# Performance work log

Measured on AMD Instinct MI355X. Metric: run time of the kernel, lower is better.

The kernel has to match this reference:

```python
import jax, jax.numpy as jnp
import numpy as np

C = 256
NH = 8
G = 32  # groupnorm groups (min(32, C))
EPS = 1e-6


def setup_inputs() -> dict:
    key = jax.random.key(0)
    ks = jax.random.split(key, 7)
    B, D, H, W = 2, 16, 16, 16
    x = jax.random.normal(ks[0], (B, C, D, H, W), dtype=jnp.float32)
    gn_gamma = jnp.ones((C,), jnp.float32)
    gn_beta = jnp.zeros((C,), jnp.float32)
    s = 1.0 / np.sqrt(C)
    qkv_w = jax.random.normal(ks[1], (3 * C, C), jnp.float32) * s  # 1x1x1 conv weight
    qkv_b = jnp.zeros((3 * C,), jnp.float32)
    proj_w = jax.random.normal(ks[2], (C, C), jnp.float32) * s
    proj_b = jnp.zeros((C,), jnp.float32)
    return {"x": x, "gn_gamma": gn_gamma, "gn_beta": gn_beta,
            "qkv_w": qkv_w, "qkv_b": qkv_b, "proj_w": proj_w, "proj_b": proj_b}


def _group_norm(x, gamma, beta):
    # x: [B, C, S]
    B, Cc, S = x.shape
    xg = x.reshape(B, G, (Cc // G) * S)
    mu = xg.mean(axis=-1, keepdims=True)
    var = xg.var(axis=-1, keepdims=True)
    xg = (xg - mu) * jax.lax.rsqrt(var + EPS)
    x = xg.reshape(B, Cc, S)
    return x * gamma[None, :, None] + beta[None, :, None]


def reference(x, gn_gamma, gn_beta, qkv_w, qkv_b, proj_w, proj_b):
    B, Cc, D, H, W = x.shape
    S = D * H * W
    hd = Cc // NH
    xf = x.reshape(B, Cc, S)
    h = _group_norm(xf, gn_gamma, gn_beta)
    # 1x1x1 conv == channel matmul: [B, 3C, S]
    qkv = jnp.einsum('oc,bcs->bos', qkv_w, h) + qkv_b[None, :, None]
    # torch path: reshape(B,3C,S).permute(0,2,1).chunk -> q=channels[0:C]
    q, k, v = qkv[:, :Cc], qkv[:, Cc:2 * Cc], qkv[:, 2 * Cc:]
    # [B, C, S] -> [B, NH, S, hd]
    def to_heads(t):
        return t.reshape(B, NH, hd, S).transpose(0, 1, 3, 2)
    q, k, v = to_heads(q), to_heads(k), to_heads(v)
    scale = hd ** (-0.5)
    attn = jax.nn.softmax(jnp.einsum('bnqd,bnkd->bnqk', q, k) * scale, axis=-1)
    o = jnp.einsum('bnqk,bnkd->bnqd', attn, v)  # [B, NH, S, hd]
    o = o.transpose(0, 1, 3, 2).reshape(B, Cc, S)  # back to [B, C, S]
    o = jnp.einsum('oc,bcs->bos', proj_w, o) + proj_b[None, :, None]
    return x + o.reshape(B, Cc, D, H, W)
```

## Files before the change

kernel.cpp:

```cpp
#include <hip/hip_runtime.h>
#include <cstddef>

#define S_LEN 4096
#define C_DIM 256
#define NHEADS 8
#define HDIM 32

typedef __attribute__((ext_vector_type(8))) _Float16 half8;
typedef __attribute__((ext_vector_type(4))) _Float16 half4;
typedef __attribute__((ext_vector_type(2))) _Float16 h2t;
typedef __attribute__((ext_vector_type(2))) __fp16 fp16x2;
typedef __attribute__((ext_vector_type(4))) float floatx4;

#define SC2F ((float)(0.17677669529663687 * 1.4426950408889634))

__global__ __launch_bounds__(256) void prep_stats(
    const float* __restrict__ qkv_w, const float* __restrict__ proj_w,
    const float* __restrict__ qkv_b, const float* __restrict__ x,
    _Float16* __restrict__ wq, _Float16* __restrict__ wp,
    float* __restrict__ qbias, float* __restrict__ pstat)
{
  const int blk = blockIdx.x;
  const int tid = threadIdx.x;
  if (blk < 512) {
    __shared__ float red[2][4];
    const int gb = blk >> 3, e = blk & 7;
    const int g = gb & 31, b = gb >> 5;
    const float* xb = x + ((size_t)b * C_DIM + g * 8) * S_LEN + e * 4096;
    const float4* x4 = (const float4*)xb;
    float sum = 0.f, sumsq = 0.f;
    #pragma unroll
    for (int i = 0; i < 4; ++i) {
      float4 v = x4[tid + i * 256];
      sum += v.x + v.y + v.z + v.w;
      sumsq += v.x * v.x + v.y * v.y + v.z * v.z + v.w * v.w;
    }
    for (int off = 1; off < 64; off <<= 1) {
      sum += __shfl_xor(sum, off, 64);
      sumsq += __shfl_xor(sumsq, off, 64);
    }
    const int wv = tid >> 6, lane = tid & 63;
    if (lane == 0) { red[0][wv] = sum; red[1][wv] = sumsq; }
    __syncthreads();
    if (tid == 0) {
      pstat[(gb * 8 + e) * 2 + 0] = red[0][0] + red[0][1] + red[0][2] + red[0][3];
      pstat[(gb * 8 + e) * 2 + 1] = red[1][0] + red[1][1] + red[1][2] + red[1][3];
    }
  } else if (blk < 704) {
    const int i = (blk - 512) * 1024 + tid * 4;
    float4 v = *(const float4*)(qkv_w + i);
    const float sc = (i < 65536) ? SC2F : 1.f;
    half4 h = { (_Float16)(v.x * sc), (_Float16)(v.y * sc),
                (_Float16)(v.z * sc), (_Float16)(v.w * sc) };
    *(half4*)(wq + i) = h;
  } else if (blk < 768) {
    const int i = (blk - 704) * 1024 + tid * 4;
    float4 v = *(const float4*)(proj_w + i);
    half4 h = { (_Float16)v.x, (_Float16)v.y, (_Float16)v.z, (_Float16)v.w };
    *(half4*)(wp + i) = h;
  } else {
    #pragma unroll
    for (int j = 0; j < 3; ++j) {
      const int i = tid + j * 256;
      float bv = qkv_b[i];
      if (i < 256) bv *= SC2F;
      qbias[i] = bv;
    }
  }
}

__global__ __launch_bounds__(256) void xnorm(
    const float* __restrict__ x, const float* __restrict__ gamma,
    const float* __restrict__ beta, const float* __restrict__ pstat,
    _Float16* __restrict__ xt)
{
  __shared__ _Float16 Lt[16][264];
  const int tid = threadIdx.x;
  const int b = blockIdx.y;
  const int s0 = blockIdx.x * 16;
  const int c = tid;
  const int gb = b * 32 + (c >> 3);
  float s = 0.f, sq = 0.f;
  #pragma unroll
  for (int e = 0; e < 8; ++e) {
    s  += pstat[(gb * 8 + e) * 2 + 0];
    sq += pstat[(gb * 8 + e) * 2 + 1];
  }
  const float mean = s * (1.f / 32768.f);
  const float rstd = rsqrtf(sq * (1.f / 32768.f) - mean * mean + 1e-6f);
  const float ga = gamma[c] * rstd, be = beta[c] - mean * ga;
  const float4* xa = (const float4*)(x + ((size_t)b * C_DIM + c) * S_LEN + s0);
  #pragma unroll
  for (int i = 0; i < 4; ++i) {
    float4 v = xa[i];
    Lt[i * 4 + 0][c] = (_Float16)(v.x * ga + be);
    Lt[i * 4 + 1][c] = (_Float16)(v.y * ga + be);
    Lt[i * 4 + 2][c] = (_Float16)(v.z * ga + be);
    Lt[i * 4 + 3][c] = (_Float16)(v.w * ga + be);
  }
  __syncthreads();
  const int sl = tid >> 4, cc = (tid & 15) * 16;
  _Float16* dst = xt + ((size_t)b * S_LEN + s0 + sl) * C_DIM + cc;
  const _Float16* src = &Lt[sl][cc];
  *(half8*)(dst + 0) = *(const half8*)(src + 0);
  *(half8*)(dst + 8) = *(const half8*)(src + 8);
}

__global__ __launch_bounds__(256) void qkv_gemm(
    const _Float16* __restrict__ W, const float* __restrict__ bias,
    const _Float16* __restrict__ xt,
    _Float16* __restrict__ qo, _Float16* __restrict__ ko_,
    _Float16* __restrict__ vo)
{
  __shared__ __align__(16) _Float16 Ld[256 * 72];
  const int tid = threadIdx.x;
  const int b = blockIdx.z;
  const int s0 = blockIdx.y * 64;

  {
    const int sl = tid >> 2, cc = (tid & 3) * 64;
    const _Float16* src = xt + ((size_t)b * S_LEN + s0 + sl) * C_DIM + cc;
    _Float16* dst = &Ld[sl * 264 + cc];
    #pragma unroll
    for (int j = 0; j < 8; ++j)
      *(half8*)(dst + j * 8) = *(const half8*)(src + j * 8);
  }
  __syncthreads();

  const int lane = tid & 63, wv = tid >> 6;
  const int m = lane & 15, quad = lane >> 4;
  const int mtb = blockIdx.x * 16 + wv * 4;
  const _Float16* wrow[4];
  #pragma unroll
  for (int j = 0; j < 4; ++j)
    wrow[j] = W + (size_t)((mtb + j) * 16 + m) * C_DIM + quad * 8;
  const _Float16* lp = &Ld[m * 264 + quad * 8];

  floatx4 acc[4][4];
  #pragma unroll
  for (int j = 0; j < 4; ++j)
    #pragma unroll
    for (int s = 0; s < 4; ++s) acc[j][s] = (floatx4){0.f,0.f,0.f,0.f};

  #pragma unroll 2
  for (int k0 = 0; k0 < C_DIM; k0 += 32) {
    half8 b0 = *(const half8*)(lp + k0);
    half8 b1 = *(const half8*)(lp + 16 * 264 + k0);
    half8 b2 = *(const half8*)(lp + 32 * 264 + k0);
    half8 b3 = *(const half8*)(lp + 48 * 264 + k0);
    #pragma unroll
    for (int j = 0; j < 4; ++j) {
      half8 a = *(const half8*)(wrow[j] + k0);
      acc[j][0] = __builtin_amdgcn_mfma_f32_16x16x32_f16(a, b0, acc[j][0], 0, 0, 0);
      acc[j][1] = __builtin_amdgcn_mfma_f32_16x16x32_f16(a, b1, acc[j][1], 0, 0, 0);
      acc[j][2] = __builtin_amdgcn_mfma_f32_16x16x32_f16(a, b2, acc[j][2], 0, 0, 0);
      acc[j][3] = __builtin_amdgcn_mfma_f32_16x16x32_f16(a, b3, acc[j][3], 0, 0, 0);
    }
  }

  if (blockIdx.x < 2) {
    #pragma unroll
    for (int j = 0; j < 4; ++j) {
      const int ob = (mtb + j) * 16 + quad * 4;
      const float bv0 = bias[ob], bv1 = bias[ob + 1],
                  bv2 = bias[ob + 2], bv3 = bias[ob + 3];
      _Float16* dst = (ob < 256) ? qo : ko_;
      const int oo = ob & 255, n = oo >> 5, d0 = oo & 31;
      #pragma unroll
      for (int sub = 0; sub < 4; ++sub) {
        int s = s0 + sub * 16 + m;
        half4 h = { (_Float16)(acc[j][sub][0] + bv0), (_Float16)(acc[j][sub][1] + bv1),
                    (_Float16)(acc[j][sub][2] + bv2), (_Float16)(acc[j][sub][3] + bv3) };
        *(half4*)(dst + (((size_t)b * NHEADS + n) * S_LEN + s) * HDIM + d0) = h;
      }
    }
  } else {
    __syncthreads();
    _Float16* VLd = Ld;
    #pragma unroll
    for (int j = 0; j < 4; ++j) {
      const int ob = (mtb + j) * 16 + quad * 4;
      const int lch = (wv * 4 + j) * 16 + quad * 4;
      const float bv0 = bias[ob], bv1 = bias[ob + 1],
                  bv2 = bias[ob + 2], bv3 = bias[ob + 3];
      #pragma unroll
      for (int sub = 0; sub < 4; ++sub) {
        int s = sub * 16 + m;
        VLd[(lch + 0) * 72 + s] = (_Float16)(acc[j][sub][0] + bv0);
        VLd[(lch + 1) * 72 + s] = (_Float16)(acc[j][sub][1] + bv1);
        VLd[(lch + 2) * 72 + s] = (_Float16)(acc[j][sub][2] + bv2);
        VLd[(lch + 3) * 72 + s] = (_Float16)(acc[j][sub][3] + bv3);
      }
    }
    __syncthreads();
    const int sh3 = tid & 7, chl = tid >> 3;
    #pragma unroll
    for (int p = 0; p < 8; ++p) {
      const int ch = p * 32 + chl;
      const int n = ch >> 5, d = ch & 31;
      _Float16* dst = vo + ((size_t)(b * NHEADS + n) * HDIM + d) * S_LEN + s0 + sh3 * 8;
      *(half8*)dst = *(const half8*)(VLd + ch * 72 + sh3 * 8);
    }
  }
}

__global__ __launch_bounds__(512) void attn_kernel(
    const _Float16* __restrict__ q, const _Float16* __restrict__ k,
    const _Float16* __restrict__ v, _Float16* __restrict__ o)
{
  __shared__ __align__(16) _Float16 Kl[2][128 * 40];
  __shared__ __align__(16) _Float16 Vl[2][32 * 136];
  const int tid = threadIdx.x;
  const int lane = tid & 63, wv = tid >> 6;
  const int m = lane & 15, quad = lane >> 4;
  const int n = blockIdx.y, b = blockIdx.z;
  const int qc = blockIdx.x;
  const int q0 = qc * 256 + wv * 32;
  const int bh = b * NHEADS + n;

  const _Float16* qb = q + (size_t)bh * S_LEN * HDIM;
  const _Float16* kb = k + (size_t)bh * S_LEN * HDIM;
  const _Float16* vb = v + (size_t)bh * HDIM * S_LEN;

  half8 qfA = *(const half8*)(qb + (size_t)(q0 + m) * HDIM + quad * 8);
  half8 qfB = *(const half8*)(qb + (size_t)(q0 + 16 + m) * HDIM + quad * 8);

  const int krow = wv * 16 + (lane >> 2), kc = (lane & 3) * 8;
  const int vrow = wv * 4 + (lane >> 4), vc = (lane & 15) * 8;
  const _Float16* kg = kb + (size_t)krow * HDIM + kc;
  const _Float16* vg = vb + (size_t)vrow * S_LEN + vc;
  const int klds = krow * 40 + kc;
  const int vlds = vrow * 136 + vc;

  int4 kreg = *(const int4*)kg;
  int4 vreg = *(const int4*)vg;
  const _Float16* kgp = kg + 128 * HDIM;
  const _Float16* vgp = vg + 128;

  floatx4 oA0 = {0.f,0.f,0.f,0.f}, oA1 = oA0, oB0 = oA0, oB1 = oA0;
  float lA0 = 0.f, lA1 = 0.f, lB0 = 0.f, lB1 = 0.f;
  const fp16x2 one2 = { (__fp16)1.0f, (__fp16)1.0f };
  const floatx4 zz = {0.f,0.f,0.f,0.f};

  #pragma unroll 2
  for (int it = 0; it < 32; ++it) {
    const int bufi = it & 1;
    *(int4*)(&Kl[bufi][klds]) = kreg;
    *(int4*)(&Vl[bufi][vlds]) = vreg;
    kreg = *(const int4*)kgp; kgp += 128 * HDIM;
    vreg = *(const int4*)vgp; vgp += 128;
    __syncthreads();
    const _Float16* Kb = Kl[bufi];
    const _Float16* Vb = Vl[bufi];

    #pragma unroll
    for (int t = 0; t < 8; ++t) {
      const int tt = (t + wv) & 7;
      half8 kf  = *(const half8*)(Kb + (tt * 16 + m) * 40 + quad * 8);
      half4 vf0 = *(const half4*)(Vb + m * 136 + tt * 16 + quad * 4);
      half4 vf1 = *(const half4*)(Vb + (16 + m) * 136 + tt * 16 + quad * 4);
      __builtin_amdgcn_s_setprio(1);
      floatx4 sA = __builtin_amdgcn_mfma_f32_16x16x32_f16(kf, qfA, zz, 0, 0, 0);
      floatx4 sB = __builtin_amdgcn_mfma_f32_16x16x32_f16(kf, qfB, zz, 0, 0, 0);
      __builtin_amdgcn_s_setprio(0);
      float eA0 = __builtin_amdgcn_exp2f(sA[0]);
      float eA1 = __builtin_amdgcn_exp2f(sA[1]);
      float eA2 = __builtin_amdgcn_exp2f(sA[2]);
      float eA3 = __builtin_amdgcn_exp2f(sA[3]);
      float eB0 = __builtin_amdgcn_exp2f(sB[0]);
      float eB1 = __builtin_amdgcn_exp2f(sB[1]);
      float eB2 = __builtin_amdgcn_exp2f(sB[2]);
      float eB3 = __builtin_amdgcn_exp2f(sB[3]);
      half4 pA, pB;
      fp16x2 pAlo = __builtin_amdgcn_cvt_pkrtz(eA0, eA1);
      fp16x2 pAhi = __builtin_amdgcn_cvt_pkrtz(eA2, eA3);
      fp16x2 pBlo = __builtin_amdgcn_cvt_pkrtz(eB0, eB1);
      fp16x2 pBhi = __builtin_amdgcn_cvt_pkrtz(eB2, eB3);
      *(fp16x2*)&pA = pAlo; *((fp16x2*)&pA + 1) = pAhi;
      *(fp16x2*)&pB = pBlo; *((fp16x2*)&pB + 1) = pBhi;
      lA0 = __builtin_amdgcn_fdot2(pAlo, one2, lA0, false);
      lA1 = __builtin_amdgcn_fdot2(pAhi, one2, lA1, false);
      lB0 = __builtin_amdgcn_fdot2(pBlo, one2, lB0, false);
      lB1 = __builtin_amdgcn_fdot2(pBhi, one2, lB1, false);
      __builtin_amdgcn_s_setprio(1);
      oA0 = __builtin_amdgcn_mfma_f32_16x16x16f16(vf0, pA, oA0, 0, 0, 0);
      oA1 = __builtin_amdgcn_mfma_f32_16x16x16f16(vf1, pA, oA1, 0, 0, 0);
      oB0 = __builtin_amdgcn_mfma_f32_16x16x16f16(vf0, pB, oB0, 0, 0, 0);
      oB1 = __builtin_amdgcn_mfma_f32_16x16x16f16(vf1, pB, oB1, 0, 0, 0);
      __builtin_amdgcn_s_setprio(0);
    }
  }
  float lA = lA0 + lA1, lB = lB0 + lB1;
  lA += __shfl_xor(lA, 16, 64); lA += __shfl_xor(lA, 32, 64);
  lB += __shfl_xor(lB, 16, 64); lB += __shfl_xor(lB, 32, 64);
  const float rA = 1.f / lA, rB = 1.f / lB;
  _Float16* obase = o + ((size_t)bh * S_LEN) * HDIM;
  {
    _Float16* oh = obase + (size_t)(q0 + m) * HDIM;
    half4 h0 = { (_Float16)(oA0[0] * rA), (_Float16)(oA0[1] * rA),
                 (_Float16)(oA0[2] * rA), (_Float16)(oA0[3] * rA) };
    half4 h1 = { (_Float16)(oA1[0] * rA), (_Float16)(oA1[1] * rA),
                 (_Float16)(oA1[2] * rA), (_Float16)(oA1[3] * rA) };
    *(half4*)(oh + quad * 4) = h0;
    *(half4*)(oh + 16 + quad * 4) = h1;
  }
  {
    _Float16* oh = obase + (size_t)(q0 + 16 + m) * HDIM;
    half4 h0 = { (_Float16)(oB0[0] * rB), (_Float16)(oB0[1] * rB),
                 (_Float16)(oB0[2] * rB), (_Float16)(oB0[3] * rB) };
    half4 h1 = { (_Float16)(oB1[0] * rB), (_Float16)(oB1[1] * rB),
                 (_Float16)(oB1[2] * rB), (_Float16)(oB1[3] * rB) };
    *(half4*)(oh + quad * 4) = h0;
    *(half4*)(oh + 16 + quad * 4) = h1;
  }
}

__global__ __launch_bounds__(256) void proj_gemm(
    const _Float16* __restrict__ W, const float* __restrict__ bias,
    const _Float16* __restrict__ o,
    const float* __restrict__ x, float* __restrict__ out)
{
  const int tid = threadIdx.x;
  const int lane = tid & 63, wv = tid >> 6;
  const int m = lane & 15, quad = lane >> 4;
  const int mtb = blockIdx.x * 8 + wv * 2;
  const int s0 = blockIdx.y * 64;
  const int b = blockIdx.z;

  const _Float16* wrow0 = W + (size_t)((mtb + 0) * 16 + m) * C_DIM + quad * 8;
  const _Float16* wrow1 = W + (size_t)((mtb + 1) * 16 + m) * C_DIM + quad * 8;
  floatx4 acc[2][4];
  #pragma unroll
  for (int j = 0; j < 2; ++j)
    #pragma unroll
    for (int s = 0; s < 4; ++s) acc[j][s] = (floatx4){0.f,0.f,0.f,0.f};

  #pragma unroll
  for (int k0 = 0; k0 < C_DIM; k0 += 32) {
    const int n = k0 >> 5;
    const int d0 = quad * 8;
    half8 bf[4];
    #pragma unroll
    for (int sub = 0; sub < 4; ++sub) {
      size_t idx = (((size_t)(b * NHEADS + n)) * S_LEN + s0 + sub * 16 + m) * HDIM + d0;
      bf[sub] = *(const half8*)(o + idx);
    }
    half8 af0 = *(const half8*)(wrow0 + k0);
    half8 af1 = *(const half8*)(wrow1 + k0);
    #pragma unroll
    for (int sub = 0; sub < 4; ++sub) {
      acc[0][sub] = __builtin_amdgcn_mfma_f32_16x16x32_f16(af0, bf[sub], acc[0][sub], 0, 0, 0);
      acc[1][sub] = __builtin_amdgcn_mfma_f32_16x16x32_f16(af1, bf[sub], acc[1][sub], 0, 0, 0);
    }
  }
  #pragma unroll
  for (int j = 0; j < 2; ++j)
    #pragma unroll
    for (int sub = 0; sub < 4; ++sub) {
      int s = s0 + sub * 16 + m;
      #pragma unroll
      for (int r = 0; r < 4; ++r) {
        int c = (mtb + j) * 16 + quad * 4 + r;
        size_t idx = ((size_t)b * C_DIM + c) * S_LEN + s;
        out[idx] = x[idx] + acc[j][sub][r] + bias[c];
      }
    }
}

extern "C" void kernel_launch(void* const* d_in, const int* in_sizes, int n_in,
                              void* d_out, int out_size, void* d_ws, size_t ws_size,
                              hipStream_t stream) {
  const float* x        = (const float*)d_in[0];
  const float* gn_gamma = (const float*)d_in[1];
  const float* gn_beta  = (const float*)d_in[2];
  const float* qkv_w    = (const float*)d_in[3];
  const float* qkv_b    = (const float*)d_in[4];
  const float* proj_w   = (const float*)d_in[5];
  const float* proj_b   = (const float*)d_in[6];
  float* out = (float*)d_out;

  const size_t n1 = (size_t)2 * S_LEN * C_DIM;
  char* ws = (char*)d_ws;
  _Float16* qx  = (_Float16*)ws;
  _Float16* kx  = qx + n1;
  _Float16* vx  = kx + n1;
  _Float16* wq  = vx + n1;
  _Float16* wp  = wq + 768 * 256;
  float*    qbias = (float*)(wp + 256 * 256);
  float*    pstat = qbias + 768;
  _Float16* ox  = (_Float16*)(pstat + 1024);
  _Float16* xt  = ox + n1;

  prep_stats<<<769, 256, 0, stream>>>(qkv_w, proj_w, qkv_b, x, wq, wp, qbias, pstat);
  xnorm<<<dim3(256, 2), 256, 0, stream>>>(x, gn_gamma, gn_beta, pstat, xt);
  qkv_gemm<<<dim3(3, 64, 2), 256, 0, stream>>>(wq, qbias, xt, qx, kx, vx);
  attn_kernel<<<dim3(16, 8, 2), 512, 0, stream>>>(qx, kx, vx, ox);
  proj_gemm<<<dim3(2, 64, 2), 256, 0, stream>>>(wp, proj_b, ox, x, out);
}
```

Measured before the change: 144.3 us.

## Fuse group-norm normalization into the QKV GEMM and drop the xt buffer

Removes the separate xnorm kernel. The QKV GEMM now reads fp32 x directly, applies the group-norm scale and shift, and writes the fp16 tile into LDS. Each 512-thread block computes all 768 output channels for 32 positions, instead of splitting Q/K/V across blocks for 64 positions. This saves one launch and the round trip of the transposed fp16 activation through global memory. In exchange, every block re-reads the whole weight matrix from L2, the grid has fewer blocks, and x is loaded with a strided per-channel pattern.

```diff
diff --git a/kernel.cpp b/kernel.cpp
--- a/kernel.cpp
+++ b/kernel.cpp
@@ -69,138 +69,113 @@
   }
 }
 
-__global__ __launch_bounds__(256) void xnorm(
+__global__ __launch_bounds__(512) void qkv_gn_gemm(
+    const _Float16* __restrict__ W, const float* __restrict__ bias,
     const float* __restrict__ x, const float* __restrict__ gamma,
     const float* __restrict__ beta, const float* __restrict__ pstat,
-    _Float16* __restrict__ xt)
-{
-  __shared__ _Float16 Lt[16][264];
-  const int tid = threadIdx.x;
-  const int b = blockIdx.y;
-  const int s0 = blockIdx.x * 16;
-  const int c = tid;
-  const int gb = b * 32 + (c >> 3);
-  float s = 0.f, sq = 0.f;
-  #pragma unroll
-  for (int e = 0; e < 8; ++e) {
-    s  += pstat[(gb * 8 + e) * 2 + 0];
-    sq += pstat[(gb * 8 + e) * 2 + 1];
-  }
-  const float mean = s * (1.f / 32768.f);
-  const float rstd = rsqrtf(sq * (1.f / 32768.f) - mean * mean + 1e-6f);
-  const float ga = gamma[c] * rstd, be = beta[c] - mean * ga;
-  const float4* xa = (const float4*)(x + ((size_t)b * C_DIM + c) * S_LEN + s0);
-  #pragma unroll
-  for (int i = 0; i < 4; ++i) {
-    float4 v = xa[i];
-    Lt[i * 4 + 0][c] = (_Float16)(v.x * ga + be);
-    Lt[i * 4 + 1][c] = (_Float16)(v.y * ga + be);
-    Lt[i * 4 + 2][c] = (_Float16)(v.z * ga + be);
-    Lt[i * 4 + 3][c] = (_Float16)(v.w * ga + be);
-  }
-  __syncthreads();
-  const int sl = tid >> 4, cc = (tid & 15) * 16;
-  _Float16* dst = xt + ((size_t)b * S_LEN + s0 + sl) * C_DIM + cc;
-  const _Float16* src = &Lt[sl][cc];
-  *(half8*)(dst + 0) = *(const half8*)(src + 0);
-  *(half8*)(dst + 8) = *(const half8*)(src + 8);
-}
-
-__global__ __launch_bounds__(256) void qkv_gemm(
-    const _Float16* __restrict__ W, const float* __restrict__ bias,
-    const _Float16* __restrict__ xt,
     _Float16* __restrict__ qo, _Float16* __restrict__ ko_,
     _Float16* __restrict__ vo)
 {
-  __shared__ __align__(16) _Float16 Ld[256 * 72];
+  __shared__ __align__(16) _Float16 Ld[256 * 40];
   const int tid = threadIdx.x;
-  const int b = blockIdx.z;
-  const int s0 = blockIdx.y * 64;
+  const int b = blockIdx.y;
+  const int s0 = blockIdx.x * 32;
 
   {
-    const int sl = tid >> 2, cc = (tid & 3) * 64;
-    const _Float16* src = xt + ((size_t)b * S_LEN + s0 + sl) * C_DIM + cc;
-    _Float16* dst = &Ld[sl * 264 + cc];
-    #pragma unroll
-    for (int j = 0; j < 8; ++j)
-      *(half8*)(dst + j * 8) = *(const half8*)(src + j * 8);
+    const int c0 = (tid & 127) * 2, c1 = c0 + 1;
+    const int sh = tid >> 7;
+    const int gb = b * 32 + (c0 >> 3);
+    float s = 0.f, sq = 0.f;
+    #pragma unroll
+    for (int e = 0; e < 8; ++e) {
+      s  += pstat[(gb * 8 + e) * 2 + 0];
+      sq += pstat[(gb * 8 + e) * 2 + 1];
+    }
+    const float mean = s * (1.f / 32768.f);
+    const float rstd = rsqrtf(sq * (1.f / 32768.f) - mean * mean + 1e-6f);
+    const float ga0 = gamma[c0] * rstd, be0 = beta[c0] - mean * ga0;
+    const float ga1 = gamma[c1] * rstd, be1 = beta[c1] - mean * ga1;
+    const float4* xa = (const float4*)(x + ((size_t)b * C_DIM + c0) * S_LEN + s0 + sh * 8);
+    const float4* xc = (const float4*)(x + ((size_t)b * C_DIM + c1) * S_LEN + s0 + sh * 8);
+    #pragma unroll
+    for (int j = 0; j < 2; ++j) {
+      float4 a = xa[j], c = xc[j];
+      int sl = sh * 8 + j * 4;
+      *(h2t*)&Ld[(sl + 0) * 264 + c0] = (h2t){ (_Float16)(a.x * ga0 + be0), (_Float16)(c.x * ga1 + be1) };
+      *(h2t*)&Ld[(sl + 1) * 264 + c0] = (h2t){ (_Float16)(a.y * ga0 + be0), (_Float16)(c.y * ga1 + be1) };
+      *(h2t*)&Ld[(sl + 2) * 264 + c0] = (h2t){ (_Float16)(a.z * ga0 + be0), (_Float16)(c.z * ga1 + be1) };
+      *(h2t*)&Ld[(sl + 3) * 264 + c0] = (h2t){ (_Float16)(a.w * ga0 + be0), (_Float16)(c.w * ga1 + be1) };
+    }
   }
   __syncthreads();
 
   const int lane = tid & 63, wv = tid >> 6;
   const int m = lane & 15, quad = lane >> 4;
-  const int mtb = blockIdx.x * 16 + wv * 4;
-  const _Float16* wrow[4];
-  #pragma unroll
-  for (int j = 0; j < 4; ++j)
-    wrow[j] = W + (size_t)((mtb + j) * 16 + m) * C_DIM + quad * 8;
+  const _Float16* wrow[6];
+  #pragma unroll
+  for (int j = 0; j < 6; ++j)
+    wrow[j] = W + (size_t)((wv + 8 * j) * 16 + m) * C_DIM + quad * 8;
   const _Float16* lp = &Ld[m * 264 + quad * 8];
 
-  floatx4 acc[4][4];
-  #pragma unroll
-  for (int j = 0; j < 4; ++j)
-    #pragma unroll
-    for (int s = 0; s < 4; ++s) acc[j][s] = (floatx4){0.f,0.f,0.f,0.f};
+  floatx4 acc[6][2];
+  #pragma unroll
+  for (int j = 0; j < 6; ++j) {
+    acc[j][0] = (floatx4){0.f,0.f,0.f,0.f};
+    acc[j][1] = (floatx4){0.f,0.f,0.f,0.f};
+  }
 
   #pragma unroll 2
   for (int k0 = 0; k0 < C_DIM; k0 += 32) {
     half8 b0 = *(const half8*)(lp + k0);
     half8 b1 = *(const half8*)(lp + 16 * 264 + k0);
-    half8 b2 = *(const half8*)(lp + 32 * 264 + k0);
-    half8 b3 = *(const half8*)(lp + 48 * 264 + k0);
-    #pragma unroll
-    for (int j = 0; j < 4; ++j) {
+    #pragma unroll
+    for (int j = 0; j < 6; ++j) {
       half8 a = *(const half8*)(wrow[j] + k0);
       acc[j][0] = __builtin_amdgcn_mfma_f32_16x16x32_f16(a, b0, acc[j][0], 0, 0, 0);
       acc[j][1] = __builtin_amdgcn_mfma_f32_16x16x32_f16(a, b1, acc[j][1], 0, 0, 0);
-      acc[j][2] = __builtin_amdgcn_mfma_f32_16x16x32_f16(a, b2, acc[j][2], 0, 0, 0);
-      acc[j][3] = __builtin_amdgcn_mfma_f32_16x16x32_f16(a, b3, acc[j][3], 0, 0, 0);
-    }
-  }
-
-  if (blockIdx.x < 2) {
-    #pragma unroll
-    for (int j = 0; j < 4; ++j) {
-      const int ob = (mtb + j) * 16 + quad * 4;
-      const float bv0 = bias[ob], bv1 = bias[ob + 1],
-                  bv2 = bias[ob + 2], bv3 = bias[ob + 3];
-      _Float16* dst = (ob < 256) ? qo : ko_;
-      const int oo = ob & 255, n = oo >> 5, d0 = oo & 31;
-      #pragma unroll
-      for (int sub = 0; sub < 4; ++sub) {
-        int s = s0 + sub * 16 + m;
-        half4 h = { (_Float16)(acc[j][sub][0] + bv0), (_Float16)(acc[j][sub][1] + bv1),
-                    (_Float16)(acc[j][sub][2] + bv2), (_Float16)(acc[j][sub][3] + bv3) };
-        *(half4*)(dst + (((size_t)b * NHEADS + n) * S_LEN + s) * HDIM + d0) = h;
-      }
-    }
-  } else {
-    __syncthreads();
-    _Float16* VLd = Ld;
-    #pragma unroll
-    for (int j = 0; j < 4; ++j) {
-      const int ob = (mtb + j) * 16 + quad * 4;
-      const int lch = (wv * 4 + j) * 16 + quad * 4;
-      const float bv0 = bias[ob], bv1 = bias[ob + 1],
-                  bv2 = bias[ob + 2], bv3 = bias[ob + 3];
-      #pragma unroll
-      for (int sub = 0; sub < 4; ++sub) {
-        int s = sub * 16 + m;
-        VLd[(lch + 0) * 72 + s] = (_Float16)(acc[j][sub][0] + bv0);
-        VLd[(lch + 1) * 72 + s] = (_Float16)(acc[j][sub][1] + bv1);
-        VLd[(lch + 2) * 72 + s] = (_Float16)(acc[j][sub][2] + bv2);
-        VLd[(lch + 3) * 72 + s] = (_Float16)(acc[j][sub][3] + bv3);
-      }
-    }
-    __syncthreads();
-    const int sh3 = tid & 7, chl = tid >> 3;
-    #pragma unroll
-    for (int p = 0; p < 8; ++p) {
-      const int ch = p * 32 + chl;
-      const int n = ch >> 5, d = ch & 31;
-      _Float16* dst = vo + ((size_t)(b * NHEADS + n) * HDIM + d) * S_LEN + s0 + sh3 * 8;
-      *(half8*)dst = *(const half8*)(VLd + ch * 72 + sh3 * 8);
-    }
+    }
+  }
+
+  __syncthreads();
+  #pragma unroll
+  for (int j = 0; j < 4; ++j) {
+    const int ob = (wv + 8 * j) * 16 + quad * 4;
+    const float bv0 = bias[ob], bv1 = bias[ob + 1],
+                bv2 = bias[ob + 2], bv3 = bias[ob + 3];
+    _Float16* dst = (ob < 256) ? qo : ko_;
+    const int oo = ob & 255, n = oo >> 5, d0 = oo & 31;
+    #pragma unroll
+    for (int sub = 0; sub < 2; ++sub) {
+      int s = s0 + sub * 16 + m;
+      half4 h = { (_Float16)(acc[j][sub][0] + bv0), (_Float16)(acc[j][sub][1] + bv1),
+                  (_Float16)(acc[j][sub][2] + bv2), (_Float16)(acc[j][sub][3] + bv3) };
+      *(half4*)(dst + (((size_t)b * NHEADS + n) * S_LEN + s) * HDIM + d0) = h;
+    }
+  }
+  _Float16* VLd = Ld;
+  #pragma unroll
+  for (int j = 4; j < 6; ++j) {
+    const int ob = (wv + 8 * j) * 16 + quad * 4;
+    const int lch = ob - 512;
+    const float bv0 = bias[ob], bv1 = bias[ob + 1],
+                bv2 = bias[ob + 2], bv3 = bias[ob + 3];
+    #pragma unroll
+    for (int sub = 0; sub < 2; ++sub) {
+      int s = sub * 16 + m;
+      VLd[(lch + 0) * 40 + s] = (_Float16)(acc[j][sub][0] + bv0);
+      VLd[(lch + 1) * 40 + s] = (_Float16)(acc[j][sub][1] + bv1);
+      VLd[(lch + 2) * 40 + s] = (_Float16)(acc[j][sub][2] + bv2);
+      VLd[(lch + 3) * 40 + s] = (_Float16)(acc[j][sub][3] + bv3);
+    }
+  }
+  __syncthreads();
+  {
+    const int ch = tid >> 1, sh = tid & 1;
+    const int n = ch >> 5, d = ch & 31;
+    _Float16* dst = vo + ((size_t)(b * NHEADS + n) * HDIM + d) * S_LEN + s0 + sh * 16;
+    const _Float16* src = VLd + ch * 40 + sh * 16;
+    *(half8*)(dst + 0) = *(const half8*)(src + 0);
+    *(half8*)(dst + 8) = *(const half8*)(src + 8);
   }
 }
 
@@ -389,11 +364,9 @@
   float*    qbias = (float*)(wp + 256 * 256);
   float*    pstat = qbias + 768;
   _Float16* ox  = (_Float16*)(pstat + 1024);
-  _Float16* xt  = ox + n1;
 
   prep_stats<<<769, 256, 0, stream>>>(qkv_w, proj_w, qkv_b, x, wq, wp, qbias, pstat);
-  xnorm<<<dim3(256, 2), 256, 0, stream>>>(x, gn_gamma, gn_beta, pstat, xt);
-  qkv_gemm<<<dim3(3, 64, 2), 256, 0, stream>>>(wq, qbias, xt, qx, kx, vx);
+  qkv_gn_gemm<<<dim3(128, 2), 512, 0, stream>>>(wq, qbias, x, gn_gamma, gn_beta, pstat, qx, kx, vx);
   attn_kernel<<<dim3(16, 8, 2), 512, 0, stream>>>(qx, kx, vx, ox);
   proj_gemm<<<dim3(2, 64, 2), 256, 0, stream>>>(wp, proj_b, ox, x, out);
 }
```

Measured after the change: 144.6 us. About the same (+0.2%).
